# Kernel optimization log

Measured on AMD Instinct MI355X. Metric: run time of the kernel, lower is better.

The kernel has to match this reference:

```python
import jax, jax.numpy as jnp
import numpy as np

NUM_USERS = 100_000
NUM_ITEMS = 50_000
DIM = 64
N_INTERACTIONS = 2_000_000  # symmetric nnz = 4M


def setup_inputs() -> dict:
    rng = np.random.default_rng(0)
    u = rng.integers(0, NUM_USERS, N_INTERACTIONS)
    it = rng.integers(0, NUM_ITEMS, N_INTERACTIONS) + NUM_USERS  # items offset by num_users
    rows = np.concatenate([u, it]).astype(np.int32)  # symmetric adjacency
    cols = np.concatenate([it, u]).astype(np.int32)
    n_nodes = NUM_USERS + NUM_ITEMS
    deg = np.bincount(rows, minlength=n_nodes).astype(np.float32)
    deg = np.maximum(deg, 1.0)
    # LightGCN symmetric normalization: A_hat[i,j] = 1/sqrt(deg_i * deg_j)
    vals = (1.0 / np.sqrt(deg[rows] * deg[cols])).astype(np.float32)

    key = jax.random.key(0)
    k1, k2 = jax.random.split(key)
    user_emb = jax.random.normal(k1, (NUM_USERS, DIM), jnp.float32) * 0.1
    item_emb = jax.random.normal(k2, (NUM_ITEMS, DIM), jnp.float32) * 0.1
    return {
        "user_emb": user_emb,
        "item_emb": item_emb,
        "rows": jnp.asarray(rows),
        "cols": jnp.asarray(cols),
        "vals": jnp.asarray(vals),
        "n_layers": 3,
    }


def reference(user_emb, item_emb, rows, cols, vals, n_layers):
    num_users = user_emb.shape[0]
    n_nodes = num_users + item_emb.shape[0]
    emb = jnp.concatenate([user_emb, item_emb], axis=0)  # [N, D]
    acc = emb
    cur = emb
    for _ in range(n_layers):
        # SpMM: cur = A_hat @ cur, via edge gather + weighted segment reduction
        msgs = vals[:, None] * cur[cols]  # [nnz, D]
        cur = jax.ops.segment_sum(msgs, rows, num_segments=n_nodes)
        acc = acc + cur
    all_emb = acc / (n_layers + 1)  # mean over [e0, e1, ..., eL]
    return all_emb[:num_users], all_emb[num_users:]
```

## Files before the change

kernel.cpp:

```cpp
#include <hip/hip_runtime.h>
#include <hip/hip_fp16.h>

#define D 64
#define NLAYERS 3
#define CHUNK 8192
#define RPB 256
#define NBMAX 640
#define NCHMAX 512
#define STAGE_CAP 8704
#define NPH 10

typedef float vfloat4 __attribute__((ext_vector_type(4)));

__global__ void init_concat(const float* __restrict__ ue, const float* __restrict__ ie,
                            const float* __restrict__ invsq,
                            __half* __restrict__ w0,
                            int n_user_elems, int n_total_elems) {
    int i4 = (blockIdx.x * blockDim.x + threadIdx.x) * 4;
    if (i4 >= n_total_elems) return;
    float4 v;
    if (i4 < n_user_elems) v = *(const float4*)(ue + i4);
    else                   v = *(const float4*)(ie + (i4 - n_user_elems));
    float isr = invsq[i4 >> 6];
    __half2 h01 = __floats2half2_rn(isr * v.x, isr * v.y);
    __half2 h23 = __floats2half2_rn(isr * v.z, isr * v.w);
    float2 packed;
    *(__half2*)&packed.x = h01;
    *(__half2*)&packed.y = h23;
    *(float2*)(w0 + i4) = packed;
}

__global__ void partition_edges(const int* __restrict__ rows, const int* __restrict__ cols,
                                int* __restrict__ gsorted, int* __restrict__ goff_c,
                                int nnz, int nb) {
    __shared__ int staged[CHUNK];
    __shared__ int cnt[NBMAX];
    __shared__ int cur[NBMAX];
    __shared__ int partial[256];
    int t = threadIdx.x;
    int base = blockIdx.x * CHUNK;

    for (int j = t; j <= nb; j += 256) cnt[j] = 0;
    __syncthreads();
    for (int k = 0; k < CHUNK; k += 256) {
        int e = base + k + t;
        if (e < nnz) atomicAdd(&cnt[rows[e] >> 8], 1);
    }
    __syncthreads();
    int i0 = t * 3, i1 = i0 + 1, i2 = i0 + 2;
    int v0 = (i0 < nb) ? cnt[i0] : 0;
    int v1 = (i1 < nb) ? cnt[i1] : 0;
    int v2 = (i2 < nb) ? cnt[i2] : 0;
    partial[t] = v0 + v1 + v2;
    __syncthreads();
    for (int off = 1; off < 256; off <<= 1) {
        int x = (t >= off) ? partial[t - off] : 0;
        __syncthreads();
        partial[t] += x;
        __syncthreads();
    }
    int excl = (t == 0) ? 0 : partial[t - 1];
    if (i0 <= nb) cnt[i0] = excl;
    if (i1 <= nb) cnt[i1] = excl + v0;
    if (i2 <= nb) cnt[i2] = excl + v0 + v1;
    __syncthreads();
    for (int j = t; j < nb; j += 256) cur[j] = cnt[j];
    __syncthreads();
    for (int k = 0; k < CHUNK; k += 256) {
        int e = base + k + t;
        if (e < nnz) {
            int r = rows[e];
            int pos = atomicAdd(&cur[r >> 8], 1);
            staged[pos] = ((r & 255) << 18) | cols[e];
        }
    }
    __syncthreads();
    int total = cnt[nb];
    for (int i = t; i < total; i += 256) gsorted[base + i] = staged[i];
    for (int j = t; j <= nb; j += 256) goff_c[blockIdx.x * (nb + 1) + j] = cnt[j];
}

__global__ void transpose_off(const int* __restrict__ goff_c, int* __restrict__ T,
                              int nch, int nbp1) {
    int c = blockIdx.x * 256 + threadIdx.x;
    int j = blockIdx.y;
    if (c < nch) T[j * nch + c] = goff_c[c * nbp1 + j];
}

__global__ void bucket_totals(const int* __restrict__ T, int* __restrict__ btot, int nch) {
    int b = blockIdx.x;
    int lane = threadIdx.x;
    int s = 0;
    for (int c = lane; c < nch; c += 64)
        s += T[(size_t)(b + 1) * nch + c] - T[(size_t)b * nch + c];
    for (int off = 32; off; off >>= 1) s += __shfl_down(s, off, 64);
    if (lane == 0) btot[b] = s;
}

__global__ void scan_buckets(const int* __restrict__ btot, int* __restrict__ bb,
                             int nb) {
    __shared__ int partial[256];
    int t = threadIdx.x;
    int i0 = t * 3, i1 = i0 + 1, i2 = i0 + 2;
    int v0 = (i0 < nb) ? btot[i0] : 0;
    int v1 = (i1 < nb) ? btot[i1] : 0;
    int v2 = (i2 < nb) ? btot[i2] : 0;
    partial[t] = v0 + v1 + v2;
    __syncthreads();
    for (int off = 1; off < 256; off <<= 1) {
        int x = (t >= off) ? partial[t - off] : 0;
        __syncthreads();
        partial[t] += x;
        __syncthreads();
    }
    int excl = (t == 0) ? 0 : partial[t - 1];
    if (i0 <= nb) bb[i0] = excl;
    if (i1 <= nb) bb[i1] = excl + v0;
    if (i2 <= nb) bb[i2] = excl + v0 + v1;
}

__global__ __launch_bounds__(256)
void csr_build_bucket(const int* __restrict__ T, const int* __restrict__ gsorted,
                      const int* __restrict__ bb,
                      int4* __restrict__ rdesc, float* __restrict__ invsq,
                      int* __restrict__ ci, int nch, int n_nodes) {
    __shared__ int staged[STAGE_CAP];
    __shared__ int sbeg[NCHMAX];
    __shared__ int slen[NCHMAX];
    __shared__ int soff[NCHMAX];
    __shared__ int pcnt[RPB * NPH];
    __shared__ int scanb[256];
    int t = threadIdx.x;
    int b = blockIdx.x;
    for (int j = t; j < nch; j += 256) {
        int s0 = T[(size_t)b * nch + j];
        int s1 = T[(size_t)(b + 1) * nch + j];
        sbeg[j] = s0;
        slen[j] = s1 - s0;
    }
    for (int j = t; j < RPB * NPH; j += 256) pcnt[j] = 0;
    __syncthreads();
    int i0 = 2 * t, i1 = 2 * t + 1;
    int l0 = (i0 < nch) ? slen[i0] : 0;
    int l1 = (i1 < nch) ? slen[i1] : 0;
    scanb[t] = l0 + l1;
    __syncthreads();
    for (int off = 1; off < 256; off <<= 1) {
        int x = (t >= off) ? scanb[t - off] : 0;
        __syncthreads();
        scanb[t] += x;
        __syncthreads();
    }
    int texcl = scanb[t] - (l0 + l1);
    if (i0 < nch) soff[i0] = texcl;
    if (i1 < nch) soff[i1] = texcl + l0;
    int total = scanb[255];
    __syncthreads();

    int w = t >> 6, lane = t & 63;
    int sub = lane >> 4, l16 = lane & 15;
    bool fits = (total <= STAGE_CAP);
    if (fits) {
        for (int c = (w << 2) + sub; c < nch; c += 16) {
            const int* seg = gsorted + (size_t)c * CHUNK + sbeg[c];
            int L = slen[c], o = soff[c];
            for (int i = l16; i < L; i += 16) staged[o + i] = seg[i];
        }
        __syncthreads();
        for (int i = t; i < total; i += 256) {
            int p = staged[i];
            atomicAdd(&pcnt[(p >> 18) * NPH + ((p & 0x3FFFF) >> 14)], 1);
        }
    } else {
        for (int c = (w << 2) + sub; c < nch; c += 16) {
            const int* seg = gsorted + (size_t)c * CHUNK + sbeg[c];
            int L = slen[c];
            for (int i = l16; i < L; i += 16) {
                int p = seg[i];
                atomicAdd(&pcnt[(p >> 18) * NPH + ((p & 0x3FFFF) >> 14)], 1);
            }
        }
    }
    __syncthreads();
    int v = 0;
    #pragma unroll
    for (int q = 0; q < NPH; ++q) v += pcnt[t * NPH + q];
    scanb[t] = v;
    __syncthreads();
    for (int off = 1; off < 256; off <<= 1) {
        int x = (t >= off) ? scanb[t - off] : 0;
        __syncthreads();
        scanb[t] += x;
        __syncthreads();
    }
    int excl = scanb[t] - v;
    int base = bb[b];
    int grow = (b << 8) + t;
    int rbeg = base + excl;
    if (grow < n_nodes) {
        float d = (float)v;
        float isr = rsqrtf(d < 1.f ? 1.f : d);
        invsq[grow] = isr;
        int4 rd;
        rd.x = rbeg;
        rd.y = rbeg + v;
        rd.z = __float_as_int(isr);
        rd.w = 0;
        rdesc[grow] = rd;
    }
    int running = rbeg;
    #pragma unroll
    for (int q = 0; q < NPH; ++q) {
        int c = pcnt[t * NPH + q];
        pcnt[t * NPH + q] = running;
        running += c;
    }
    __syncthreads();
    if (fits) {
        for (int i = t; i < total; i += 256) {
            int p = staged[i];
            int c = p & 0x3FFFF;
            int pos = atomicAdd(&pcnt[(p >> 18) * NPH + (c >> 14)], 1);
            ci[pos] = c;
        }
    } else {
        for (int c = (w << 2) + sub; c < nch; c += 16) {
            const int* seg = gsorted + (size_t)c * CHUNK + sbeg[c];
            int L = slen[c];
            for (int i = l16; i < L; i += 16) {
                int p = seg[i];
                int cc = p & 0x3FFFF;
                int pos = atomicAdd(&pcnt[(p >> 18) * NPH + (cc >> 14)], 1);
                ci[pos] = cc;
            }
        }
    }
}

__global__ __launch_bounds__(256)
void spmm_gather(const int4* __restrict__ rdesc, const int* __restrict__ ci,
                 const __half* __restrict__ xh,
                 __half* __restrict__ ynext,
                 const __half* __restrict__ opA,
                 const float* __restrict__ ue, const float* __restrict__ ie,
                 float* __restrict__ outp,
                 int n_user, int n_nodes, int last) {
    int wid  = (blockIdx.x * blockDim.x + threadIdx.x) >> 6;
    int lane = threadIdx.x & 63;
    if (wid >= n_nodes) return;
    int sub = lane >> 4;
    int d4  = (lane & 15) << 2;
    int4 rd = rdesc[wid];
    int beg = rd.x, end = rd.y;
    float isr = __int_as_float(rd.z);

    float4 b4;
    float2 q1, q2;
    if (last && sub == 0) {
        size_t o = ((size_t)wid << 6) + d4;
        const float* eb = (wid < n_user) ? (ue + o)
                                         : (ie + o - ((size_t)n_user << 6));
        b4 = *(const float4*)eb;
        q1 = *(const float2*)(opA + o);
        q2 = *(const float2*)(xh + o);
    }

    __half2 z = __floats2half2_rn(0.f, 0.f);
    __half2 a01 = z, a23 = z, b01 = z, b23 = z;
    __half2 c01 = z, c23 = z, d01 = z, d23 = z;
    int e = beg + sub;
    for (; e + 12 < end; e += 16) {
        int k0 = __builtin_nontemporal_load(ci + e);
        int k1 = __builtin_nontemporal_load(ci + e + 4);
        int k2 = __builtin_nontemporal_load(ci + e + 8);
        int k3 = __builtin_nontemporal_load(ci + e + 12);
        float2 r0 = *(const float2*)(xh + ((size_t)k0 << 6) + d4);
        float2 r1 = *(const float2*)(xh + ((size_t)k1 << 6) + d4);
        float2 r2 = *(const float2*)(xh + ((size_t)k2 << 6) + d4);
        float2 r3 = *(const float2*)(xh + ((size_t)k3 << 6) + d4);
        a01 = __hadd2(a01, *(__half2*)&r0.x); a23 = __hadd2(a23, *(__half2*)&r0.y);
        b01 = __hadd2(b01, *(__half2*)&r1.x); b23 = __hadd2(b23, *(__half2*)&r1.y);
        c01 = __hadd2(c01, *(__half2*)&r2.x); c23 = __hadd2(c23, *(__half2*)&r2.y);
        d01 = __hadd2(d01, *(__half2*)&r3.x); d23 = __hadd2(d23, *(__half2*)&r3.y);
    }
    for (; e + 4 < end; e += 8) {
        int k0 = __builtin_nontemporal_load(ci + e);
        int k1 = __builtin_nontemporal_load(ci + e + 4);
        float2 r0 = *(const float2*)(xh + ((size_t)k0 << 6) + d4);
        float2 r1 = *(const float2*)(xh + ((size_t)k1 << 6) + d4);
        a01 = __hadd2(a01, *(__half2*)&r0.x); a23 = __hadd2(a23, *(__half2*)&r0.y);
        b01 = __hadd2(b01, *(__half2*)&r1.x); b23 = __hadd2(b23, *(__half2*)&r1.y);
    }
    if (e < end) {
        int k0 = ci[e];
        float2 r0 = *(const float2*)(xh + ((size_t)k0 << 6) + d4);
        a01 = __hadd2(a01, *(__half2*)&r0.x); a23 = __hadd2(a23, *(__half2*)&r0.y);
    }
    float2 fa = __half22float2(a01), fb = __half22float2(b01);
    float2 fc = __half22float2(c01), fd = __half22float2(d01);
    float sx = (fa.x + fb.x) + (fc.x + fd.x);
    float sy = (fa.y + fb.y) + (fc.y + fd.y);
    fa = __half22float2(a23); fb = __half22float2(b23);
    fc = __half22float2(c23); fd = __half22float2(d23);
    float sz = (fa.x + fb.x) + (fc.x + fd.x);
    float sw = (fa.y + fb.y) + (fc.y + fd.y);
    sx += __shfl_xor(sx, 16, 64); sy += __shfl_xor(sy, 16, 64);
    sz += __shfl_xor(sz, 16, 64); sw += __shfl_xor(sw, 16, 64);
    sx += __shfl_xor(sx, 32, 64); sy += __shfl_xor(sy, 32, 64);
    sz += __shfl_xor(sz, 32, 64); sw += __shfl_xor(sw, 32, 64);

    if (sub == 0) {
        size_t o = ((size_t)wid << 6) + d4;
        float cx = isr * sx, cy = isr * sy, cz = isr * sz, cw = isr * sw;
        if (last) {
            float sd = 1.0f / isr;
            float2 f1a = __half22float2(*(__half2*)&q1.x);
            float2 f1b = __half22float2(*(__half2*)&q1.y);
            float2 f2a = __half22float2(*(__half2*)&q2.x);
            float2 f2b = __half22float2(*(__half2*)&q2.y);
            vfloat4 o4;
            o4.x = (b4.x + (f1a.x + f2a.x) * sd + cx) * 0.25f;
            o4.y = (b4.y + (f1a.y + f2a.y) * sd + cy) * 0.25f;
            o4.z = (b4.z + (f1b.x + f2b.x) * sd + cz) * 0.25f;
            o4.w = (b4.w + (f1b.y + f2b.y) * sd + cw) * 0.25f;
            __builtin_nontemporal_store(o4, (vfloat4*)(outp + o));
        } else {
            __half2 h01 = __floats2half2_rn(isr * cx, isr * cy);
            __half2 h23 = __floats2half2_rn(isr * cz, isr * cw);
            float2 packed;
            *(__half2*)&packed.x = h01;
            *(__half2*)&packed.y = h23;
            *(float2*)(ynext + o) = packed;
        }
    }
}

extern "C" void kernel_launch(void* const* d_in, const int* in_sizes, int n_in,
                              void* d_out, int out_size, void* d_ws, size_t ws_size,
                              hipStream_t stream) {
    const float* ue   = (const float*)d_in[0];
    const float* ie   = (const float*)d_in[1];
    const int*   rows = (const int*)d_in[2];
    const int*   cols = (const int*)d_in[3];

    const int n_user_elems  = in_sizes[0];
    const int n_total_elems = out_size;
    const int n_nodes       = n_total_elems / D;
    const int n_user        = n_user_elems / D;
    const int nnz           = in_sizes[2];

    const int nb  = (n_nodes + RPB - 1) / RPB;
    const int nch = (nnz + CHUNK - 1) / CHUNK;

    float* out = (float*)d_out;

    char* w = (char*)d_ws;
    __half* w0h    = (__half*)w; w += (size_t)n_total_elems * 2;
    __half* w1h    = (__half*)w; w += (size_t)n_total_elems * 2;
    int*   gsorted = (int*)w;    w += (size_t)nch * CHUNK * 4;
    int*   ci      = (int*)w;    w += (size_t)nnz * 4;
    float* invsq   = (float*)w;  w += (size_t)n_nodes * 4;
    int4*  rdesc   = (int4*)w;   w += ((size_t)n_nodes + 16) * 16;
    int*   goff_c  = (int*)w;    w += (size_t)nch * (nb + 1) * 4;
    int*   Tt      = (int*)w;    w += (size_t)(nb + 1) * nch * 4;
    int*   btot    = (int*)w;    w += (size_t)(nb + 16) * 4;
    int*   bb      = (int*)w;    w += (size_t)(nb + 16) * 4;

    partition_edges<<<nch, 256, 0, stream>>>(rows, cols, gsorted, goff_c, nnz, nb);
    dim3 tg((nch + 255) / 256, nb + 1);
    transpose_off<<<tg, 256, 0, stream>>>(goff_c, Tt, nch, nb + 1);
    bucket_totals<<<nb, 64, 0, stream>>>(Tt, btot, nch);
    scan_buckets<<<1, 256, 0, stream>>>(btot, bb, nb);
    csr_build_bucket<<<nb, 256, 0, stream>>>(Tt, gsorted, bb, rdesc, invsq, ci, nch, n_nodes);

    const int elem_blocks = (n_total_elems / 4 + 255) / 256;
    init_concat<<<elem_blocks, 256, 0, stream>>>(ue, ie, invsq, w0h,
                                                 n_user_elems, n_total_elems);

    __half* cur = w0h;
    __half* nxt = w1h;
    const int blocks = (n_nodes * 64 + 255) / 256;
    for (int l = 0; l < NLAYERS; ++l) {
        int last = (l == NLAYERS - 1);
        spmm_gather<<<blocks, 256, 0, stream>>>(rdesc, ci, cur, nxt,
                                                w1h, ue, ie, out,
                                                n_user, n_nodes, last);
        __half* t = cur; cur = nxt; nxt = t;
    }
}
```

Baseline: 489.9 us.

## Pad CSR rows to multiples of eight and assign sixteen lanes per row

Each CSR row is padded to a multiple of 8 entries, and the padding points at an extra zero row appended to both half-precision embedding buffers. This lets the SpMM kernel use one 16-lane group per node, with vectorized int4 index loads and no remainder loops or cross-subgroup shuffles. Four times as many rows now run per wavefront and no lanes sit idle at the write stage. In exchange, memory traffic goes up from the padded dummy gathers, and each lane serially walks the whole row, which lengthens the dependency chain on high-degree nodes.

```diff
diff --git a/kernel.cpp b/kernel.cpp
--- a/kernel.cpp
+++ b/kernel.cpp
@@ -9,15 +9,24 @@
 #define NCHMAX 512
 #define STAGE_CAP 8704
 #define NPH 10
+#define PADSLOT 2048
 
 typedef float vfloat4 __attribute__((ext_vector_type(4)));
+typedef int   vint4   __attribute__((ext_vector_type(4)));
 
 __global__ void init_concat(const float* __restrict__ ue, const float* __restrict__ ie,
                             const float* __restrict__ invsq,
-                            __half* __restrict__ w0,
+                            __half* __restrict__ w0, __half* __restrict__ w1,
                             int n_user_elems, int n_total_elems) {
     int i4 = (blockIdx.x * blockDim.x + threadIdx.x) * 4;
-    if (i4 >= n_total_elems) return;
+    if (i4 >= n_total_elems) {
+        if (i4 < n_total_elems + 64) {
+            float2 zz; zz.x = 0.f; zz.y = 0.f;
+            *(float2*)(w0 + i4) = zz;
+            *(float2*)(w1 + i4) = zz;
+        }
+        return;
+    }
     float4 v;
     if (i4 < n_user_elems) v = *(const float4*)(ue + i4);
     else                   v = *(const float4*)(ie + (i4 - n_user_elems));
@@ -185,7 +194,8 @@
     int v = 0;
     #pragma unroll
     for (int q = 0; q < NPH; ++q) v += pcnt[t * NPH + q];
-    scanb[t] = v;
+    int v_pad = (v + 7) & ~7;
+    scanb[t] = v_pad;
     __syncthreads();
     for (int off = 1; off < 256; off <<= 1) {
         int x = (t >= off) ? scanb[t - off] : 0;
@@ -193,8 +203,8 @@
         scanb[t] += x;
         __syncthreads();
     }
-    int excl = scanb[t] - v;
-    int base = bb[b];
+    int excl = scanb[t] - v_pad;
+    int base = bb[b] + (b << 11);
     int grow = (b << 8) + t;
     int rbeg = base + excl;
     if (grow < n_nodes) {
@@ -203,10 +213,11 @@
         invsq[grow] = isr;
         int4 rd;
         rd.x = rbeg;
-        rd.y = rbeg + v;
+        rd.y = rbeg + v_pad;
         rd.z = __float_as_int(isr);
         rd.w = 0;
         rdesc[grow] = rd;
+        for (int i = v; i < v_pad; ++i) ci[rbeg + i] = n_nodes;
     }
     int running = rbeg;
     #pragma unroll
@@ -245,93 +256,75 @@
                  const float* __restrict__ ue, const float* __restrict__ ie,
                  float* __restrict__ outp,
                  int n_user, int n_nodes, int last) {
-    int wid  = (blockIdx.x * blockDim.x + threadIdx.x) >> 6;
-    int lane = threadIdx.x & 63;
+    int tid = blockIdx.x * blockDim.x + threadIdx.x;
+    int wid = tid >> 4;
     if (wid >= n_nodes) return;
-    int sub = lane >> 4;
-    int d4  = (lane & 15) << 2;
+    int d4 = (threadIdx.x & 15) << 2;
     int4 rd = rdesc[wid];
     int beg = rd.x, end = rd.y;
     float isr = __int_as_float(rd.z);
 
-    float4 b4;
-    float2 q1, q2;
-    if (last && sub == 0) {
-        size_t o = ((size_t)wid << 6) + d4;
-        const float* eb = (wid < n_user) ? (ue + o)
-                                         : (ie + o - ((size_t)n_user << 6));
+    size_t o = ((size_t)wid << 6) + d4;
+    float4 b4; float2 q1, q2;
+    if (last) {
+        const float* eb = (wid < n_user) ? (ue + o) : (ie + o - ((size_t)n_user << 6));
         b4 = *(const float4*)eb;
         q1 = *(const float2*)(opA + o);
         q2 = *(const float2*)(xh + o);
     }
 
+    const __half* xl = xh + d4;
     __half2 z = __floats2half2_rn(0.f, 0.f);
-    __half2 a01 = z, a23 = z, b01 = z, b23 = z;
-    __half2 c01 = z, c23 = z, d01 = z, d23 = z;
-    int e = beg + sub;
-    for (; e + 12 < end; e += 16) {
-        int k0 = __builtin_nontemporal_load(ci + e);
-        int k1 = __builtin_nontemporal_load(ci + e + 4);
-        int k2 = __builtin_nontemporal_load(ci + e + 8);
-        int k3 = __builtin_nontemporal_load(ci + e + 12);
-        float2 r0 = *(const float2*)(xh + ((size_t)k0 << 6) + d4);
-        float2 r1 = *(const float2*)(xh + ((size_t)k1 << 6) + d4);
-        float2 r2 = *(const float2*)(xh + ((size_t)k2 << 6) + d4);
-        float2 r3 = *(const float2*)(xh + ((size_t)k3 << 6) + d4);
-        a01 = __hadd2(a01, *(__half2*)&r0.x); a23 = __hadd2(a23, *(__half2*)&r0.y);
-        b01 = __hadd2(b01, *(__half2*)&r1.x); b23 = __hadd2(b23, *(__half2*)&r1.y);
-        c01 = __hadd2(c01, *(__half2*)&r2.x); c23 = __hadd2(c23, *(__half2*)&r2.y);
-        d01 = __hadd2(d01, *(__half2*)&r3.x); d23 = __hadd2(d23, *(__half2*)&r3.y);
-    }
-    for (; e + 4 < end; e += 8) {
-        int k0 = __builtin_nontemporal_load(ci + e);
-        int k1 = __builtin_nontemporal_load(ci + e + 4);
-        float2 r0 = *(const float2*)(xh + ((size_t)k0 << 6) + d4);
-        float2 r1 = *(const float2*)(xh + ((size_t)k1 << 6) + d4);
-        a01 = __hadd2(a01, *(__half2*)&r0.x); a23 = __hadd2(a23, *(__half2*)&r0.y);
-        b01 = __hadd2(b01, *(__half2*)&r1.x); b23 = __hadd2(b23, *(__half2*)&r1.y);
-    }
-    if (e < end) {
-        int k0 = ci[e];
-        float2 r0 = *(const float2*)(xh + ((size_t)k0 << 6) + d4);
-        a01 = __hadd2(a01, *(__half2*)&r0.x); a23 = __hadd2(a23, *(__half2*)&r0.y);
-    }
-    float2 fa = __half22float2(a01), fb = __half22float2(b01);
-    float2 fc = __half22float2(c01), fd = __half22float2(d01);
+    __half2 a0 = z, a1 = z, b0 = z, b1 = z, c0 = z, c1 = z, d0 = z, d1 = z;
+    for (int e = beg; e < end; e += 8) {
+        vint4 ka = __builtin_nontemporal_load((const vint4*)(ci + e));
+        vint4 kb = __builtin_nontemporal_load((const vint4*)(ci + e + 4));
+        float2 r0 = *(const float2*)(xl + ((size_t)ka.x << 6));
+        float2 r1 = *(const float2*)(xl + ((size_t)ka.y << 6));
+        float2 r2 = *(const float2*)(xl + ((size_t)ka.z << 6));
+        float2 r3 = *(const float2*)(xl + ((size_t)ka.w << 6));
+        float2 r4 = *(const float2*)(xl + ((size_t)kb.x << 6));
+        float2 r5 = *(const float2*)(xl + ((size_t)kb.y << 6));
+        float2 r6 = *(const float2*)(xl + ((size_t)kb.z << 6));
+        float2 r7 = *(const float2*)(xl + ((size_t)kb.w << 6));
+        a0 = __hadd2(a0, *(__half2*)&r0.x); a1 = __hadd2(a1, *(__half2*)&r0.y);
+        b0 = __hadd2(b0, *(__half2*)&r1.x); b1 = __hadd2(b1, *(__half2*)&r1.y);
+        c0 = __hadd2(c0, *(__half2*)&r2.x); c1 = __hadd2(c1, *(__half2*)&r2.y);
+        d0 = __hadd2(d0, *(__half2*)&r3.x); d1 = __hadd2(d1, *(__half2*)&r3.y);
+        a0 = __hadd2(a0, *(__half2*)&r4.x); a1 = __hadd2(a1, *(__half2*)&r4.y);
+        b0 = __hadd2(b0, *(__half2*)&r5.x); b1 = __hadd2(b1, *(__half2*)&r5.y);
+        c0 = __hadd2(c0, *(__half2*)&r6.x); c1 = __hadd2(c1, *(__half2*)&r6.y);
+        d0 = __hadd2(d0, *(__half2*)&r7.x); d1 = __hadd2(d1, *(__half2*)&r7.y);
+    }
+    float2 fa = __half22float2(a0), fb = __half22float2(b0);
+    float2 fc = __half22float2(c0), fd = __half22float2(d0);
     float sx = (fa.x + fb.x) + (fc.x + fd.x);
     float sy = (fa.y + fb.y) + (fc.y + fd.y);
-    fa = __half22float2(a23); fb = __half22float2(b23);
-    fc = __half22float2(c23); fd = __half22float2(d23);
+    fa = __half22float2(a1); fb = __half22float2(b1);
+    fc = __half22float2(c1); fd = __half22float2(d1);
     float sz = (fa.x + fb.x) + (fc.x + fd.x);
     float sw = (fa.y + fb.y) + (fc.y + fd.y);
-    sx += __shfl_xor(sx, 16, 64); sy += __shfl_xor(sy, 16, 64);
-    sz += __shfl_xor(sz, 16, 64); sw += __shfl_xor(sw, 16, 64);
-    sx += __shfl_xor(sx, 32, 64); sy += __shfl_xor(sy, 32, 64);
-    sz += __shfl_xor(sz, 32, 64); sw += __shfl_xor(sw, 32, 64);
-
-    if (sub == 0) {
-        size_t o = ((size_t)wid << 6) + d4;
-        float cx = isr * sx, cy = isr * sy, cz = isr * sz, cw = isr * sw;
-        if (last) {
-            float sd = 1.0f / isr;
-            float2 f1a = __half22float2(*(__half2*)&q1.x);
-            float2 f1b = __half22float2(*(__half2*)&q1.y);
-            float2 f2a = __half22float2(*(__half2*)&q2.x);
-            float2 f2b = __half22float2(*(__half2*)&q2.y);
-            vfloat4 o4;
-            o4.x = (b4.x + (f1a.x + f2a.x) * sd + cx) * 0.25f;
-            o4.y = (b4.y + (f1a.y + f2a.y) * sd + cy) * 0.25f;
-            o4.z = (b4.z + (f1b.x + f2b.x) * sd + cz) * 0.25f;
-            o4.w = (b4.w + (f1b.y + f2b.y) * sd + cw) * 0.25f;
-            __builtin_nontemporal_store(o4, (vfloat4*)(outp + o));
-        } else {
-            __half2 h01 = __floats2half2_rn(isr * cx, isr * cy);
-            __half2 h23 = __floats2half2_rn(isr * cz, isr * cw);
-            float2 packed;
-            *(__half2*)&packed.x = h01;
-            *(__half2*)&packed.y = h23;
-            *(float2*)(ynext + o) = packed;
-        }
+
+    float cx = isr * sx, cy = isr * sy, cz = isr * sz, cw = isr * sw;
+    if (last) {
+        float sd = 1.0f / isr;
+        float2 f1a = __half22float2(*(__half2*)&q1.x);
+        float2 f1b = __half22float2(*(__half2*)&q1.y);
+        float2 f2a = __half22float2(*(__half2*)&q2.x);
+        float2 f2b = __half22float2(*(__half2*)&q2.y);
+        vfloat4 o4;
+        o4.x = (b4.x + (f1a.x + f2a.x) * sd + cx) * 0.25f;
+        o4.y = (b4.y + (f1a.y + f2a.y) * sd + cy) * 0.25f;
+        o4.z = (b4.z + (f1b.x + f2b.x) * sd + cz) * 0.25f;
+        o4.w = (b4.w + (f1b.y + f2b.y) * sd + cw) * 0.25f;
+        __builtin_nontemporal_store(o4, (vfloat4*)(outp + o));
+    } else {
+        __half2 h01 = __floats2half2_rn(isr * cx, isr * cy);
+        __half2 h23 = __floats2half2_rn(isr * cz, isr * cw);
+        float2 packed;
+        *(__half2*)&packed.x = h01;
+        *(__half2*)&packed.y = h23;
+        *(float2*)(ynext + o) = packed;
     }
 }
 
@@ -355,10 +348,10 @@
     float* out = (float*)d_out;
 
     char* w = (char*)d_ws;
-    __half* w0h    = (__half*)w; w += (size_t)n_total_elems * 2;
-    __half* w1h    = (__half*)w; w += (size_t)n_total_elems * 2;
+    __half* w0h    = (__half*)w; w += ((size_t)n_total_elems + 64) * 2;
+    __half* w1h    = (__half*)w; w += ((size_t)n_total_elems + 64) * 2;
     int*   gsorted = (int*)w;    w += (size_t)nch * CHUNK * 4;
-    int*   ci      = (int*)w;    w += (size_t)nnz * 4;
+    int*   ci      = (int*)w;    w += ((size_t)nnz + (size_t)nb * PADSLOT + 64) * 4;
     float* invsq   = (float*)w;  w += (size_t)n_nodes * 4;
     int4*  rdesc   = (int4*)w;   w += ((size_t)n_nodes + 16) * 16;
     int*   goff_c  = (int*)w;    w += (size_t)nch * (nb + 1) * 4;
@@ -373,13 +366,13 @@
     scan_buckets<<<1, 256, 0, stream>>>(btot, bb, nb);
     csr_build_bucket<<<nb, 256, 0, stream>>>(Tt, gsorted, bb, rdesc, invsq, ci, nch, n_nodes);
 
-    const int elem_blocks = (n_total_elems / 4 + 255) / 256;
-    init_concat<<<elem_blocks, 256, 0, stream>>>(ue, ie, invsq, w0h,
+    const int elem_blocks = ((n_total_elems + 64) / 4 + 255) / 256;
+    init_concat<<<elem_blocks, 256, 0, stream>>>(ue, ie, invsq, w0h, w1h,
                                                  n_user_elems, n_total_elems);
 
     __half* cur = w0h;
     __half* nxt = w1h;
-    const int blocks = (n_nodes * 64 + 255) / 256;
+    const int blocks = (n_nodes + 15) / 16;
     for (int l = 0; l < NLAYERS; ++l) {
         int last = (l == NLAYERS - 1);
         spmm_gather<<<blocks, 256, 0, stream>>>(rdesc, ci, cur, nxt,
```

Measured after the change: 446.2 us. -8.9%, faster.
